# Kernel tuning notes

Hardware: AMD Instinct MI355X
Metric: run time of the kernel (lower is better)

The kernel has to match this reference:

```python
import jax, jax.numpy as jnp
import numpy as np

INPUT_DIM, HIDDEN_DIM, OUTPUT_DIM = 64, 256, 64
# AutoNCP(256, 64): inter_and_command=192, command=int(0.4*192)=76, inter=116, motor=64
INTER, COMMAND, MOTOR = 116, 76, 64
SENSORY_FANOUT, INTER_FANOUT, MOTOR_FANIN = 58, 38, 38
B, T = 512, 256


def setup_inputs() -> dict:
    rng = np.random.default_rng(0)
    key = jax.random.key(0)
    d = {}
    # NCP wiring sparsity (binary masks; ncps takes abs() so polarity is irrelevant for the mask)
    m0 = np.zeros((INTER, INPUT_DIM), np.float32)
    for i in range(INPUT_DIM):
        m0[rng.choice(INTER, SENSORY_FANOUT, replace=False), i] = 1.0
    m1 = np.zeros((COMMAND, INTER), np.float32)
    for i in range(INTER):
        m1[rng.choice(COMMAND, INTER_FANOUT, replace=False), i] = 1.0
    m2 = np.zeros((MOTOR, COMMAND), np.float32)
    for o in range(MOTOR):
        m2[o, rng.choice(COMMAND, MOTOR_FANIN, replace=False)] = 1.0
    dims = [(INPUT_DIM, INTER, m0), (INTER, COMMAND, m1), (COMMAND, MOTOR, m2)]
    for l, (fi, h, m) in enumerate(dims):
        cat = fi + h
        # mask shape [h, fi+h]: sparse prev-layer block + all-ones recurrent block (as in WiredCfCCell)
        d[f"mask_{l}"] = jnp.asarray(np.concatenate([m, np.ones((h, h), np.float32)], axis=1))
        bound = float(1.0 / np.sqrt(cat))
        for nm in ("ff1", "ff2", "ta", "tb"):
            key, k1, k2 = jax.random.split(key, 3)
            d[f"w_{nm}_{l}"] = jax.random.uniform(k1, (h, cat), minval=-bound, maxval=bound, dtype=jnp.float32)
            d[f"b_{nm}_{l}"] = jax.random.uniform(k2, (h,), minval=-bound, maxval=bound, dtype=jnp.float32)
    key, k1, k2, kx = jax.random.split(key, 4)
    bound = float(1.0 / np.sqrt(OUTPUT_DIM))
    d["w_fc"] = jax.random.uniform(k1, (OUTPUT_DIM, OUTPUT_DIM), minval=-bound, maxval=bound, dtype=jnp.float32)
    d["b_fc"] = jax.random.uniform(k2, (OUTPUT_DIM,), minval=-bound, maxval=bound, dtype=jnp.float32)
    d["x"] = jax.random.normal(kx, (B, T, INPUT_DIM), dtype=jnp.float32)
    return d


def _cfc_cell(xin, h, w1, b1, w2, b2, wa, ba, wb, bb, mask):
    # CfCCell 'default' mode, no backbone, ts = 1.0
    cat = jnp.concatenate([xin, h], axis=-1)          # [B, fi+h]
    ff1 = jnp.tanh(cat @ (w1 * mask).T + b1)
    ff2 = jnp.tanh(cat @ (w2 * mask).T + b2)
    t_interp = jax.nn.sigmoid(cat @ wa.T + ba + cat @ wb.T + bb)  # sigmoid(t_a*1.0 + t_b)
    return ff1 * (1.0 - t_interp) + t_interp * ff2


def _forward(x, layer_params, masks, w_fc, b_fc):
    bsz = x.shape[0]
    h0 = tuple(jnp.zeros((bsz, h), x.dtype) for h in (INTER, COMMAND, MOTOR))

    def step(hs, xt):
        inp = xt
        new = []
        for l in range(3):  # inter -> command -> motor (structurally distinct layers)
            h = _cfc_cell(inp, hs[l], *layer_params[l], masks[l])
            inp = h
            new.append(h)
        return tuple(new), inp  # motor-layer output per step

    _, ys = jax.lax.scan(step, h0, jnp.swapaxes(x, 0, 1))
    y = jnp.swapaxes(ys, 0, 1)  # [B, T, MOTOR]
    return y @ w_fc.T + b_fc


def reference(x, w_ff1_0, b_ff1_0, w_ff2_0, b_ff2_0, w_ta_0, b_ta_0, w_tb_0, b_tb_0,
              w_ff1_1, b_ff1_1, w_ff2_1, b_ff2_1, w_ta_1, b_ta_1, w_tb_1, b_tb_1,
              w_ff1_2, b_ff1_2, w_ff2_2, b_ff2_2, w_ta_2, b_ta_2, w_tb_2, b_tb_2,
              w_fc, b_fc, mask_0, mask_1, mask_2):
    layer_params = [
        (w_ff1_0, b_ff1_0, w_ff2_0, b_ff2_0, w_ta_0, b_ta_0, w_tb_0, b_tb_0),
        (w_ff1_1, b_ff1_1, w_ff2_1, b_ff2_1, w_ta_1, b_ta_1, w_tb_1, b_tb_1),
        (w_ff1_2, b_ff1_2, w_ff2_2, b_ff2_2, w_ta_2, b_ta_2, w_tb_2, b_tb_2),
    ]
    return _forward(x, layer_params, (mask_0, mask_1, mask_2), w_fc, b_fc)
```

## Files before the change

### kernel.cpp

```cpp
#include <hip/hip_runtime.h>

typedef _Float16 f16x8 __attribute__((ext_vector_type(8)));
typedef _Float16 f16x4 __attribute__((ext_vector_type(4)));
typedef _Float16 f16x2 __attribute__((ext_vector_type(2)));
typedef float f32x4 __attribute__((ext_vector_type(4)));

#define NTH 512
#define SEQT 256
#define LD0 200
#define LD1 200
#define LD2 168

struct KArgs { const float* in[30]; float* out; };

__device__ __forceinline__ float fast_tanh(float x) {
  return __fdividef(2.0f, 1.0f + __expf(-2.0f * x)) - 1.0f;
}
__device__ __forceinline__ float fast_sig(float x) {
  return __fdividef(1.0f, 1.0f + __expf(-x));
}

__device__ __forceinline__ f32x4 mfma16(f16x8 a, f16x8 b, f32x4 c) {
  return __builtin_amdgcn_mfma_f32_16x16x32_f16(a, b, c, 0, 0, 0);
}

__device__ __forceinline__ f16x4 combine3(const f32x4 acc[3]) {
  f16x4 v;
  #pragma unroll
  for (int q = 0; q < 4; ++q) {
    const float ff1 = fast_tanh(acc[0][q]);
    const float ff2 = fast_tanh(acc[1][q]);
    const float ti  = fast_sig(acc[2][q]);
    v[q] = (_Float16)(ff1 + ti * (ff2 - ff1));
  }
  return v;
}

template<int BASE, int KT>
__device__ __forceinline__ void load_tile(f16x8* wW, const float* W1, const float* W2,
                                          const float* Wa, const float* Wb,
                                          const float* Mk, int n, int CAT, int H, int kb) {
  #pragma unroll
  for (int kt = 0; kt < KT; ++kt) {
    #pragma unroll
    for (int m = 0; m < 3; ++m) {
      f16x8 f;
      #pragma unroll
      for (int j = 0; j < 8; ++j) {
        const int k = kt * 32 + kb + j;
        float v = 0.f;
        if (n < H && k < CAT) {
          if (m == 0)      v = W1[n*CAT+k] * Mk[n*CAT+k];
          else if (m == 1) v = W2[n*CAT+k] * Mk[n*CAT+k];
          else             v = Wa[n*CAT+k] + Wb[n*CAT+k];
        }
        f[j] = (_Float16)v;
      }
      wW[BASE + m*KT + kt] = f;
    }
  }
}

template<int KT>
__device__ __forceinline__ void loadB(f16x8* B, const _Float16* c, int LD, int r, int kb) {
  #pragma unroll
  for (int kt = 0; kt < KT; ++kt)
    B[kt] = *reinterpret_cast<const f16x8*>(c + r*LD + kt*32 + kb);
}

template<int BASE, int KT>
__device__ __forceinline__ void mma_tile(f32x4 acc[3], const f16x8* wW, const f16x8* B) {
  #pragma unroll
  for (int kt = 0; kt < KT; ++kt)
    #pragma unroll
    for (int m = 0; m < 3; ++m)
      acc[m] = mfma16(wW[BASE + m*KT + kt], B[kt], acc[m]);
}

__device__ __forceinline__ void init3(f32x4 acc[3], const float* sb, int bs, int n0) {
  #pragma unroll
  for (int m = 0; m < 3; ++m)
    acc[m] = *reinterpret_cast<const f32x4*>(sb + m*bs + n0);
}

__device__ __forceinline__ f16x8 loadB8u(const _Float16* p) {
  const f16x4 a = *reinterpret_cast<const f16x4*>(p);
  const f16x4 b = *reinterpret_cast<const f16x4*>(p + 4);
  f16x8 v;
  v[0]=a[0]; v[1]=a[1]; v[2]=a[2]; v[3]=a[3];
  v[4]=b[0]; v[5]=b[1]; v[6]=b[2]; v[7]=b[3];
  return v;
}

__global__ __launch_bounds__(NTH, 2) void ncp_fused(KArgs args) {
  __shared__ __align__(16) _Float16 c0[2][16 * LD0];
  __shared__ __align__(16) _Float16 c1[2][16 * LD1];
  __shared__ __align__(16) _Float16 c2[2][16 * LD2];
  __shared__ __align__(16) _Float16 wt3[15 * 64 * 8];
  __shared__ float b0s[3 * 128], b1s[3 * 80], b2s[3 * 64], bfcs[64];

  const int tid  = threadIdx.x;
  const int w    = tid >> 6;
  const int lane = tid & 63;
  const int r    = lane & 15;
  const int g    = lane >> 4;
  const int kb   = g * 8;
  const int wgBase = blockIdx.x * 16;
  const float* __restrict__ xg = args.in[29];

  f16x8 wW[37];
  if (w < 4) {
    load_tile<0, 6>(wW, args.in[1], args.in[3], args.in[5], args.in[7], args.in[0],
                    (2*w)*16 + r, 180, 116, kb);
    load_tile<18, 6>(wW, args.in[1], args.in[3], args.in[5], args.in[7], args.in[0],
                     (2*w+1)*16 + r, 180, 116, kb);
  } else if (w < 6) {
    load_tile<0, 6>(wW, args.in[10], args.in[12], args.in[14], args.in[16], args.in[9],
                    (2*(w-4))*16 + r, 192, 76, kb);
    load_tile<18, 6>(wW, args.in[10], args.in[12], args.in[14], args.in[16], args.in[9],
                     (2*(w-4)+1)*16 + r, 192, 76, kb);
  } else if (w == 6) {
    load_tile<0, 6>(wW, args.in[10], args.in[12], args.in[14], args.in[16], args.in[9],
                    64 + r, 192, 76, kb);
    load_tile<18, 5>(wW, args.in[19], args.in[21], args.in[23], args.in[25], args.in[18],
                     r, 140, 64, kb);
  } else {
    load_tile<0, 5>(wW, args.in[19], args.in[21], args.in[23], args.in[25], args.in[18],
                    16 + r, 140, 64, kb);
    load_tile<15, 5>(wW, args.in[19], args.in[21], args.in[23], args.in[25], args.in[18],
                     32 + r, 140, 64, kb);
  }
  if (w >= 6) {
    const int ot0 = (w - 6) * 2;
    #pragma unroll
    for (int tl = 0; tl < 2; ++tl)
      #pragma unroll
      for (int kt = 0; kt < 2; ++kt) {
        f16x8 f;
        #pragma unroll
        for (int j = 0; j < 8; ++j)
          f[j] = (_Float16)args.in[27][((ot0 + tl)*16 + r)*64 + kt*32 + kb + j];
        wW[33 + tl*2 + kt] = f;
      }
  }

  for (int u = tid; u < 15 * 64; u += NTH) {
    const int ln = u & 63;
    const int ff = u >> 6;
    const int kt = ff % 5, m = ff / 5;
    const int n  = 48 + (ln & 15);
    const int kbb = (ln >> 4) * 8;
    f16x8 f;
    #pragma unroll
    for (int j = 0; j < 8; ++j) {
      const int k = kt*32 + kbb + j;
      float v = 0.f;
      if (k < 140) {
        if (m == 0)      v = args.in[19][n*140+k] * args.in[18][n*140+k];
        else if (m == 1) v = args.in[21][n*140+k] * args.in[18][n*140+k];
        else             v = args.in[23][n*140+k] + args.in[25][n*140+k];
      }
      f[j] = (_Float16)v;
    }
    *reinterpret_cast<f16x8*>(wt3 + (size_t)u * 8) = f;
  }
  if (tid < 128) {
    b0s[tid]       = (tid < 116) ? args.in[2][tid] : 0.f;
    b0s[128 + tid] = (tid < 116) ? args.in[4][tid] : 0.f;
    b0s[256 + tid] = (tid < 116) ? args.in[6][tid] + args.in[8][tid] : 0.f;
  }
  if (tid < 80) {
    b1s[tid]       = (tid < 76) ? args.in[11][tid] : 0.f;
    b1s[80 + tid]  = (tid < 76) ? args.in[13][tid] : 0.f;
    b1s[160 + tid] = (tid < 76) ? args.in[15][tid] + args.in[17][tid] : 0.f;
  }
  if (tid < 64) {
    b2s[tid]       = args.in[20][tid];
    b2s[64 + tid]  = args.in[22][tid];
    b2s[128 + tid] = args.in[24][tid] + args.in[26][tid];
    bfcs[tid]      = args.in[28][tid];
  }
  for (int i = tid; i < 2 * 16 * LD0; i += NTH) c0[0][i] = (_Float16)0.f;
  for (int i = tid; i < 2 * 16 * LD1; i += NTH) c1[0][i] = (_Float16)0.f;
  for (int i = tid; i < 2 * 16 * LD2; i += NTH) c2[0][i] = (_Float16)0.f;
  __syncthreads();
  const int rr = tid >> 5, cc = (tid & 31) * 2;
  {
    const float2 v = *reinterpret_cast<const float2*>(
        xg + ((size_t)(wgBase + rr) * SEQT) * 64 + cc);
    f16x2 pk; pk[0] = (_Float16)v.x; pk[1] = (_Float16)v.y;
    *reinterpret_cast<f16x2*>(c0[0] + rr * LD0 + cc) = pk;
  }
  __syncthreads();

  const float* xp = xg + ((size_t)(wgBase + rr) * SEQT + 1) * 64 + cc;
  float* outp = args.out + ((size_t)(wgBase + r) * SEQT) * 64 + (w - 6) * 32 + 4 * g;

  #pragma unroll 1
  for (int p = 0; p < SEQT + 3; ++p) {
    const int cur = p & 1, nxt = cur ^ 1;

    float2 xv;
    const bool doX = (p < SEQT - 1);
    if (doX) xv = *reinterpret_cast<const float2*>(xp);

    if (w < 4) {
      if (p < SEQT) {
        f16x8 B[6]; loadB<6>(B, c0[cur], LD0, r, kb);
        f32x4 a[3];
        const int nA = (2*w)*16 + 4*g;
        init3(a, b0s, 128, nA);
        __builtin_amdgcn_s_setprio(1);
        mma_tile<0, 6>(a, wW, B);
        __builtin_amdgcn_s_setprio(0);
        const f16x4 vA = combine3(a);
        *reinterpret_cast<f16x4*>(c1[nxt] + r*LD1 + nA)      = vA;
        *reinterpret_cast<f16x4*>(c0[nxt] + r*LD0 + 64 + nA) = vA;
        const int nB = nA + 16;
        init3(a, b0s, 128, nB);
        __builtin_amdgcn_s_setprio(1);
        mma_tile<18, 6>(a, wW, B);
        __builtin_amdgcn_s_setprio(0);
        const f16x4 vB = combine3(a);
        if (nB < 116) {
          *reinterpret_cast<f16x4*>(c1[nxt] + r*LD1 + nB)      = vB;
          *reinterpret_cast<f16x4*>(c0[nxt] + r*LD0 + 64 + nB) = vB;
        }
      }
    } else if (w < 6) {
      if (p >= 1 && p <= SEQT) {
        f16x8 B[6]; loadB<6>(B, c1[cur], LD1, r, kb);
        f32x4 a[3];
        const int nA = (2*(w-4))*16 + 4*g;
        init3(a, b1s, 80, nA);
        __builtin_amdgcn_s_setprio(1);
        mma_tile<0, 6>(a, wW, B);
        __builtin_amdgcn_s_setprio(0);
        const f16x4 vA = combine3(a);
        *reinterpret_cast<f16x4*>(c1[nxt] + r*LD1 + 116 + nA) = vA;
        *reinterpret_cast<f16x4*>(c2[nxt] + r*LD2 + nA)       = vA;
        const int nB = nA + 16;
        init3(a, b1s, 80, nB);
        __builtin_amdgcn_s_setprio(1);
        mma_tile<18, 6>(a, wW, B);
        __builtin_amdgcn_s_setprio(0);
        const f16x4 vB = combine3(a);
        *reinterpret_cast<f16x4*>(c1[nxt] + r*LD1 + 116 + nB) = vB;
        *reinterpret_cast<f16x4*>(c2[nxt] + r*LD2 + nB)       = vB;
      }
    } else if (w == 6) {
      if (p >= 3) {
        f32x4 fa0 = *reinterpret_cast<const f32x4*>(bfcs + 4*g);
        f32x4 fa1 = *reinterpret_cast<const f32x4*>(bfcs + 16 + 4*g);
        const f16x8 hb0 = loadB8u(c2[cur] + r*LD2 + 76 + kb);
        const f16x8 hb1 = loadB8u(c2[cur] + r*LD2 + 76 + 32 + kb);
        fa0 = mfma16(wW[33], hb0, fa0); fa0 = mfma16(wW[34], hb1, fa0);
        fa1 = mfma16(wW[35], hb0, fa1); fa1 = mfma16(wW[36], hb1, fa1);
        *reinterpret_cast<f32x4*>(outp)      = fa0;
        *reinterpret_cast<f32x4*>(outp + 16) = fa1;
        outp += 64;
      }
      if (p >= 1 && p <= SEQT) {
        f16x8 B[6]; loadB<6>(B, c1[cur], LD1, r, kb);
        f32x4 a[3];
        const int n4 = 64 + 4*g;
        init3(a, b1s, 80, n4);
        __builtin_amdgcn_s_setprio(1);
        mma_tile<0, 6>(a, wW, B);
        __builtin_amdgcn_s_setprio(0);
        const f16x4 v4 = combine3(a);
        if (n4 < 76) {
          *reinterpret_cast<f16x4*>(c1[nxt] + r*LD1 + 116 + n4) = v4;
          *reinterpret_cast<f16x4*>(c2[nxt] + r*LD2 + n4)       = v4;
        }
      }
      if (p >= 2 && p <= SEQT + 1) {
        f16x8 B[5]; loadB<5>(B, c2[cur], LD2, r, kb);
        f32x4 a[3];
        const int nn = 4*g;
        init3(a, b2s, 64, nn);
        __builtin_amdgcn_s_setprio(1);
        mma_tile<18, 5>(a, wW, B);
        __builtin_amdgcn_s_setprio(0);
        const f16x4 v0 = combine3(a);
        *reinterpret_cast<f16x4*>(c2[nxt] + r*LD2 + 76 + nn) = v0;
      }
    } else {
      if (p >= 3) {
        f32x4 fa0 = *reinterpret_cast<const f32x4*>(bfcs + 32 + 4*g);
        f32x4 fa1 = *reinterpret_cast<const f32x4*>(bfcs + 48 + 4*g);
        const f16x8 hb0 = loadB8u(c2[cur] + r*LD2 + 76 + kb);
        const f16x8 hb1 = loadB8u(c2[cur] + r*LD2 + 76 + 32 + kb);
        fa0 = mfma16(wW[33], hb0, fa0); fa0 = mfma16(wW[34], hb1, fa0);
        fa1 = mfma16(wW[35], hb0, fa1); fa1 = mfma16(wW[36], hb1, fa1);
        *reinterpret_cast<f32x4*>(outp)      = fa0;
        *reinterpret_cast<f32x4*>(outp + 16) = fa1;
        outp += 64;
      }
      if (p >= 2 && p <= SEQT + 1) {
        f16x8 B[5]; loadB<5>(B, c2[cur], LD2, r, kb);
        f32x4 a[3];
        const int n1 = 16 + 4*g;
        init3(a, b2s, 64, n1);
        __builtin_amdgcn_s_setprio(1);
        mma_tile<0, 5>(a, wW, B);
        __builtin_amdgcn_s_setprio(0);
        const f16x4 v1 = combine3(a);
        *reinterpret_cast<f16x4*>(c2[nxt] + r*LD2 + 76 + n1) = v1;
        const int n2 = 32 + 4*g;
        init3(a, b2s, 64, n2);
        __builtin_amdgcn_s_setprio(1);
        mma_tile<15, 5>(a, wW, B);
        __builtin_amdgcn_s_setprio(0);
        const f16x4 v2 = combine3(a);
        *reinterpret_cast<f16x4*>(c2[nxt] + r*LD2 + 76 + n2) = v2;
        const int n3 = 48 + 4*g;
        init3(a, b2s, 64, n3);
        __builtin_amdgcn_s_setprio(1);
        #pragma unroll
        for (int kt = 0; kt < 5; ++kt) {
          #pragma unroll
          for (int m = 0; m < 3; ++m) {
            const f16x8 af = *reinterpret_cast<const f16x8*>(
                wt3 + (size_t)((m*5 + kt)*64 + lane) * 8);
            a[m] = mfma16(af, B[kt], a[m]);
          }
        }
        __builtin_amdgcn_s_setprio(0);
        const f16x4 v3 = combine3(a);
        *reinterpret_cast<f16x4*>(c2[nxt] + r*LD2 + 76 + n3) = v3;
      }
    }

    if (doX) {
      f16x2 pk; pk[0] = (_Float16)xv.x; pk[1] = (_Float16)xv.y;
      *reinterpret_cast<f16x2*>(c0[nxt] + rr * LD0 + cc) = pk;
      xp += 64;
    }
    __syncthreads();
  }
}

extern "C" void kernel_launch(void* const* d_in, const int* in_sizes, int n_in,
                              void* d_out, int out_size, void* d_ws, size_t ws_size,
                              hipStream_t stream) {
  KArgs args;
  for (int i = 0; i < 30; ++i) args.in[i] = (const float*)d_in[i];
  args.out = (float*)d_out;
  ncp_fused<<<dim3(32), dim3(NTH), 0, stream>>>(args);
}
```

Baseline: 810.9 us.

## Double workgroup to 16 waves, one output tile per wave

Raises the block size from 512 to 1024 threads so each wave computes a single 16-row output tile per layer instead of two. The per-wave register weight cache shrinks from 37 to 18 fragments, and the FC weights move into shared memory. The aim is to shorten the per-step critical path of the serial recurrence by spreading the MFMA and activation work across more waves. In exchange, each per-step barrier now synchronises twice as many waves, and the launch-bounds change raises the occupancy target.

Measured after the change: 712.7 us. 1.14x faster.

```diff
diff --git a/kernel.cpp b/kernel.cpp
--- a/kernel.cpp
+++ b/kernel.cpp
@@ -5,7 +5,7 @@
 typedef _Float16 f16x2 __attribute__((ext_vector_type(2)));
 typedef float f32x4 __attribute__((ext_vector_type(4)));
 
-#define NTH 512
+#define NTH 1024
 #define SEQT 256
 #define LD0 200
 #define LD1 200
@@ -36,7 +36,7 @@
   return v;
 }
 
-template<int BASE, int KT>
+template<int KT>
 __device__ __forceinline__ void load_tile(f16x8* wW, const float* W1, const float* W2,
                                           const float* Wa, const float* Wb,
                                           const float* Mk, int n, int CAT, int H, int kb) {
@@ -56,25 +56,22 @@
         }
         f[j] = (_Float16)v;
       }
-      wW[BASE + m*KT + kt] = f;
+      wW[m*KT + kt] = f;
     }
   }
 }
 
 template<int KT>
-__device__ __forceinline__ void loadB(f16x8* B, const _Float16* c, int LD, int r, int kb) {
-  #pragma unroll
-  for (int kt = 0; kt < KT; ++kt)
-    B[kt] = *reinterpret_cast<const f16x8*>(c + r*LD + kt*32 + kb);
-}
-
-template<int BASE, int KT>
-__device__ __forceinline__ void mma_tile(f32x4 acc[3], const f16x8* wW, const f16x8* B) {
-  #pragma unroll
-  for (int kt = 0; kt < KT; ++kt)
+__device__ __forceinline__ void mma_tile_ld(f32x4 acc[3], const f16x8* wW,
+                                            const _Float16* __restrict__ c,
+                                            int LD, int r, int kb) {
+  #pragma unroll
+  for (int kt = 0; kt < KT; ++kt) {
+    const f16x8 b = *reinterpret_cast<const f16x8*>(c + r*LD + kt*32 + kb);
     #pragma unroll
     for (int m = 0; m < 3; ++m)
-      acc[m] = mfma16(wW[BASE + m*KT + kt], B[kt], acc[m]);
+      acc[m] = mfma16(wW[m*KT + kt], b, acc[m]);
+  }
 }
 
 __device__ __forceinline__ void init3(f32x4 acc[3], const float* sb, int bs, int n0) {
@@ -92,15 +89,16 @@
   return v;
 }
 
-__global__ __launch_bounds__(NTH, 2) void ncp_fused(KArgs args) {
+__global__ __launch_bounds__(NTH, 4) void ncp_fused(KArgs args) {
   __shared__ __align__(16) _Float16 c0[2][16 * LD0];
   __shared__ __align__(16) _Float16 c1[2][16 * LD1];
   __shared__ __align__(16) _Float16 c2[2][16 * LD2];
   __shared__ __align__(16) _Float16 wt3[15 * 64 * 8];
+  __shared__ __align__(16) _Float16 wfcs[8 * 64 * 8];
   __shared__ float b0s[3 * 128], b1s[3 * 80], b2s[3 * 64], bfcs[64];
 
   const int tid  = threadIdx.x;
-  const int w    = tid >> 6;
+  const int wv   = tid >> 6;
   const int lane = tid & 63;
   const int r    = lane & 15;
   const int g    = lane >> 4;
@@ -108,40 +106,16 @@
   const int wgBase = blockIdx.x * 16;
   const float* __restrict__ xg = args.in[29];
 
-  f16x8 wW[37];
-  if (w < 4) {
-    load_tile<0, 6>(wW, args.in[1], args.in[3], args.in[5], args.in[7], args.in[0],
-                    (2*w)*16 + r, 180, 116, kb);
-    load_tile<18, 6>(wW, args.in[1], args.in[3], args.in[5], args.in[7], args.in[0],
-                     (2*w+1)*16 + r, 180, 116, kb);
-  } else if (w < 6) {
-    load_tile<0, 6>(wW, args.in[10], args.in[12], args.in[14], args.in[16], args.in[9],
-                    (2*(w-4))*16 + r, 192, 76, kb);
-    load_tile<18, 6>(wW, args.in[10], args.in[12], args.in[14], args.in[16], args.in[9],
-                     (2*(w-4)+1)*16 + r, 192, 76, kb);
-  } else if (w == 6) {
-    load_tile<0, 6>(wW, args.in[10], args.in[12], args.in[14], args.in[16], args.in[9],
-                    64 + r, 192, 76, kb);
-    load_tile<18, 5>(wW, args.in[19], args.in[21], args.in[23], args.in[25], args.in[18],
-                     r, 140, 64, kb);
+  f16x8 wW[18];
+  if (wv < 8) {
+    load_tile<6>(wW, args.in[1], args.in[3], args.in[5], args.in[7], args.in[0],
+                 wv*16 + r, 180, 116, kb);
+  } else if (wv < 13) {
+    load_tile<6>(wW, args.in[10], args.in[12], args.in[14], args.in[16], args.in[9],
+                 (wv-8)*16 + r, 192, 76, kb);
   } else {
-    load_tile<0, 5>(wW, args.in[19], args.in[21], args.in[23], args.in[25], args.in[18],
-                    16 + r, 140, 64, kb);
-    load_tile<15, 5>(wW, args.in[19], args.in[21], args.in[23], args.in[25], args.in[18],
-                     32 + r, 140, 64, kb);
-  }
-  if (w >= 6) {
-    const int ot0 = (w - 6) * 2;
-    #pragma unroll
-    for (int tl = 0; tl < 2; ++tl)
-      #pragma unroll
-      for (int kt = 0; kt < 2; ++kt) {
-        f16x8 f;
-        #pragma unroll
-        for (int j = 0; j < 8; ++j)
-          f[j] = (_Float16)args.in[27][((ot0 + tl)*16 + r)*64 + kt*32 + kb + j];
-        wW[33 + tl*2 + kt] = f;
-      }
+    load_tile<5>(wW, args.in[19], args.in[21], args.in[23], args.in[25], args.in[18],
+                 (wv-13)*16 + r, 140, 64, kb);
   }
 
   for (int u = tid; u < 15 * 64; u += NTH) {
@@ -164,6 +138,16 @@
     }
     *reinterpret_cast<f16x8*>(wt3 + (size_t)u * 8) = f;
   }
+  for (int u = tid; u < 8 * 64; u += NTH) {
+    const int ln = u & 63;
+    const int ff = u >> 6;
+    const int kt = ff & 1, ot = ff >> 1;
+    f16x8 f;
+    #pragma unroll
+    for (int j = 0; j < 8; ++j)
+      f[j] = (_Float16)args.in[27][(ot*16 + (ln & 15))*64 + kt*32 + (ln >> 4)*8 + j];
+    *reinterpret_cast<f16x8*>(wfcs + (size_t)u * 8) = f;
+  }
   if (tid < 128) {
     b0s[tid]       = (tid < 116) ? args.in[2][tid] : 0.f;
     b0s[128 + tid] = (tid < 116) ? args.in[4][tid] : 0.f;
@@ -184,8 +168,8 @@
   for (int i = tid; i < 2 * 16 * LD1; i += NTH) c1[0][i] = (_Float16)0.f;
   for (int i = tid; i < 2 * 16 * LD2; i += NTH) c2[0][i] = (_Float16)0.f;
   __syncthreads();
-  const int rr = tid >> 5, cc = (tid & 31) * 2;
-  {
+  const int rr = (tid & 511) >> 5, cc = (tid & 31) * 2;
+  if (tid < 512) {
     const float2 v = *reinterpret_cast<const float2*>(
         xg + ((size_t)(wgBase + rr) * SEQT) * 64 + cc);
     f16x2 pk; pk[0] = (_Float16)v.x; pk[1] = (_Float16)v.y;
@@ -194,141 +178,94 @@
   __syncthreads();
 
   const float* xp = xg + ((size_t)(wgBase + rr) * SEQT + 1) * 64 + cc;
-  float* outp = args.out + ((size_t)(wgBase + r) * SEQT) * 64 + (w - 6) * 32 + 4 * g;
+  const int otb = (wv >= 13) ? (wv - 13) : 0;
+  float* outp = args.out + ((size_t)(wgBase + r) * SEQT) * 64 + otb * 32 + 4 * g;
 
   #pragma unroll 1
   for (int p = 0; p < SEQT + 3; ++p) {
     const int cur = p & 1, nxt = cur ^ 1;
 
     float2 xv;
-    const bool doX = (p < SEQT - 1);
+    const bool doX = (tid < 512) && (p < SEQT - 1);
     if (doX) xv = *reinterpret_cast<const float2*>(xp);
 
-    if (w < 4) {
+    if (wv < 8) {
       if (p < SEQT) {
-        f16x8 B[6]; loadB<6>(B, c0[cur], LD0, r, kb);
         f32x4 a[3];
-        const int nA = (2*w)*16 + 4*g;
-        init3(a, b0s, 128, nA);
-        __builtin_amdgcn_s_setprio(1);
-        mma_tile<0, 6>(a, wW, B);
-        __builtin_amdgcn_s_setprio(0);
-        const f16x4 vA = combine3(a);
-        *reinterpret_cast<f16x4*>(c1[nxt] + r*LD1 + nA)      = vA;
-        *reinterpret_cast<f16x4*>(c0[nxt] + r*LD0 + 64 + nA) = vA;
-        const int nB = nA + 16;
-        init3(a, b0s, 128, nB);
-        __builtin_amdgcn_s_setprio(1);
-        mma_tile<18, 6>(a, wW, B);
-        __builtin_amdgcn_s_setprio(0);
-        const f16x4 vB = combine3(a);
-        if (nB < 116) {
-          *reinterpret_cast<f16x4*>(c1[nxt] + r*LD1 + nB)      = vB;
-          *reinterpret_cast<f16x4*>(c0[nxt] + r*LD0 + 64 + nB) = vB;
-        }
-      }
-    } else if (w < 6) {
+        const int nb = wv*16 + 4*g;
+        init3(a, b0s, 128, nb);
+        __builtin_amdgcn_s_setprio(1);
+        mma_tile_ld<6>(a, wW, c0[cur], LD0, r, kb);
+        __builtin_amdgcn_s_setprio(0);
+        const f16x4 v = combine3(a);
+        if (nb < 116) {
+          *reinterpret_cast<f16x4*>(c1[nxt] + r*LD1 + nb)      = v;
+          *reinterpret_cast<f16x4*>(c0[nxt] + r*LD0 + 64 + nb) = v;
+        }
+      }
+    } else if (wv < 13) {
       if (p >= 1 && p <= SEQT) {
-        f16x8 B[6]; loadB<6>(B, c1[cur], LD1, r, kb);
         f32x4 a[3];
-        const int nA = (2*(w-4))*16 + 4*g;
-        init3(a, b1s, 80, nA);
-        __builtin_amdgcn_s_setprio(1);
-        mma_tile<0, 6>(a, wW, B);
-        __builtin_amdgcn_s_setprio(0);
-        const f16x4 vA = combine3(a);
-        *reinterpret_cast<f16x4*>(c1[nxt] + r*LD1 + 116 + nA) = vA;
-        *reinterpret_cast<f16x4*>(c2[nxt] + r*LD2 + nA)       = vA;
-        const int nB = nA + 16;
-        init3(a, b1s, 80, nB);
-        __builtin_amdgcn_s_setprio(1);
-        mma_tile<18, 6>(a, wW, B);
-        __builtin_amdgcn_s_setprio(0);
-        const f16x4 vB = combine3(a);
-        *reinterpret_cast<f16x4*>(c1[nxt] + r*LD1 + 116 + nB) = vB;
-        *reinterpret_cast<f16x4*>(c2[nxt] + r*LD2 + nB)       = vB;
-      }
-    } else if (w == 6) {
+        const int nb = (wv-8)*16 + 4*g;
+        init3(a, b1s, 80, nb);
+        __builtin_amdgcn_s_setprio(1);
+        mma_tile_ld<6>(a, wW, c1[cur], LD1, r, kb);
+        __builtin_amdgcn_s_setprio(0);
+        const f16x4 v = combine3(a);
+        if (nb < 76) {
+          *reinterpret_cast<f16x4*>(c1[nxt] + r*LD1 + 116 + nb) = v;
+          *reinterpret_cast<f16x4*>(c2[nxt] + r*LD2 + nb)       = v;
+        }
+      }
+    } else if (wv < 15) {
       if (p >= 3) {
-        f32x4 fa0 = *reinterpret_cast<const f32x4*>(bfcs + 4*g);
-        f32x4 fa1 = *reinterpret_cast<const f32x4*>(bfcs + 16 + 4*g);
+        const int ot0 = (wv - 13) * 2;
+        f32x4 fa0 = *reinterpret_cast<const f32x4*>(bfcs + ot0*16 + 4*g);
+        f32x4 fa1 = *reinterpret_cast<const f32x4*>(bfcs + ot0*16 + 16 + 4*g);
         const f16x8 hb0 = loadB8u(c2[cur] + r*LD2 + 76 + kb);
         const f16x8 hb1 = loadB8u(c2[cur] + r*LD2 + 76 + 32 + kb);
-        fa0 = mfma16(wW[33], hb0, fa0); fa0 = mfma16(wW[34], hb1, fa0);
-        fa1 = mfma16(wW[35], hb0, fa1); fa1 = mfma16(wW[36], hb1, fa1);
+        const f16x8 wf00 = *reinterpret_cast<const f16x8*>(wfcs + (size_t)((ot0*2    )*64 + lane)*8);
+        const f16x8 wf01 = *reinterpret_cast<const f16x8*>(wfcs + (size_t)((ot0*2 + 1)*64 + lane)*8);
+        const f16x8 wf10 = *reinterpret_cast<const f16x8*>(wfcs + (size_t)((ot0*2 + 2)*64 + lane)*8);
+        const f16x8 wf11 = *reinterpret_cast<const f16x8*>(wfcs + (size_t)((ot0*2 + 3)*64 + lane)*8);
+        fa0 = mfma16(wf00, hb0, fa0); fa0 = mfma16(wf01, hb1, fa0);
+        fa1 = mfma16(wf10, hb0, fa1); fa1 = mfma16(wf11, hb1, fa1);
         *reinterpret_cast<f32x4*>(outp)      = fa0;
         *reinterpret_cast<f32x4*>(outp + 16) = fa1;
         outp += 64;
       }
-      if (p >= 1 && p <= SEQT) {
-        f16x8 B[6]; loadB<6>(B, c1[cur], LD1, r, kb);
+      if (p >= 2 && p <= SEQT + 1) {
         f32x4 a[3];
-        const int n4 = 64 + 4*g;
-        init3(a, b1s, 80, n4);
-        __builtin_amdgcn_s_setprio(1);
-        mma_tile<0, 6>(a, wW, B);
-        __builtin_amdgcn_s_setprio(0);
-        const f16x4 v4 = combine3(a);
-        if (n4 < 76) {
-          *reinterpret_cast<f16x4*>(c1[nxt] + r*LD1 + 116 + n4) = v4;
-          *reinterpret_cast<f16x4*>(c2[nxt] + r*LD2 + n4)       = v4;
-        }
-      }
+        const int nb = (wv-13)*16 + 4*g;
+        init3(a, b2s, 64, nb);
+        __builtin_amdgcn_s_setprio(1);
+        mma_tile_ld<5>(a, wW, c2[cur], LD2, r, kb);
+        __builtin_amdgcn_s_setprio(0);
+        const f16x4 v = combine3(a);
+        *reinterpret_cast<f16x4*>(c2[nxt] + r*LD2 + 76 + nb) = v;
+      }
+    } else {
       if (p >= 2 && p <= SEQT + 1) {
-        f16x8 B[5]; loadB<5>(B, c2[cur], LD2, r, kb);
-        f32x4 a[3];
-        const int nn = 4*g;
-        init3(a, b2s, 64, nn);
-        __builtin_amdgcn_s_setprio(1);
-        mma_tile<18, 5>(a, wW, B);
-        __builtin_amdgcn_s_setprio(0);
-        const f16x4 v0 = combine3(a);
-        *reinterpret_cast<f16x4*>(c2[nxt] + r*LD2 + 76 + nn) = v0;
-      }
-    } else {
-      if (p >= 3) {
-        f32x4 fa0 = *reinterpret_cast<const f32x4*>(bfcs + 32 + 4*g);
-        f32x4 fa1 = *reinterpret_cast<const f32x4*>(bfcs + 48 + 4*g);
-        const f16x8 hb0 = loadB8u(c2[cur] + r*LD2 + 76 + kb);
-        const f16x8 hb1 = loadB8u(c2[cur] + r*LD2 + 76 + 32 + kb);
-        fa0 = mfma16(wW[33], hb0, fa0); fa0 = mfma16(wW[34], hb1, fa0);
-        fa1 = mfma16(wW[35], hb0, fa1); fa1 = mfma16(wW[36], hb1, fa1);
-        *reinterpret_cast<f32x4*>(outp)      = fa0;
-        *reinterpret_cast<f32x4*>(outp + 16) = fa1;
-        outp += 64;
-      }
-      if (p >= 2 && p <= SEQT + 1) {
-        f16x8 B[5]; loadB<5>(B, c2[cur], LD2, r, kb);
-        f32x4 a[3];
-        const int n1 = 16 + 4*g;
-        init3(a, b2s, 64, n1);
-        __builtin_amdgcn_s_setprio(1);
-        mma_tile<0, 5>(a, wW, B);
-        __builtin_amdgcn_s_setprio(0);
-        const f16x4 v1 = combine3(a);
-        *reinterpret_cast<f16x4*>(c2[nxt] + r*LD2 + 76 + n1) = v1;
-        const int n2 = 32 + 4*g;
-        init3(a, b2s, 64, n2);
-        __builtin_amdgcn_s_setprio(1);
-        mma_tile<15, 5>(a, wW, B);
-        __builtin_amdgcn_s_setprio(0);
-        const f16x4 v2 = combine3(a);
-        *reinterpret_cast<f16x4*>(c2[nxt] + r*LD2 + 76 + n2) = v2;
-        const int n3 = 48 + 4*g;
-        init3(a, b2s, 64, n3);
+        f32x4 a2[3], a3[3];
+        init3(a2, b2s, 64, 32 + 4*g);
+        init3(a3, b2s, 64, 48 + 4*g);
         __builtin_amdgcn_s_setprio(1);
         #pragma unroll
         for (int kt = 0; kt < 5; ++kt) {
+          const f16x8 b = *reinterpret_cast<const f16x8*>(c2[cur] + r*LD2 + kt*32 + kb);
           #pragma unroll
           for (int m = 0; m < 3; ++m) {
+            a2[m] = mfma16(wW[m*5 + kt], b, a2[m]);
             const f16x8 af = *reinterpret_cast<const f16x8*>(
                 wt3 + (size_t)((m*5 + kt)*64 + lane) * 8);
-            a[m] = mfma16(af, B[kt], a[m]);
+            a3[m] = mfma16(af, b, a3[m]);
           }
         }
         __builtin_amdgcn_s_setprio(0);
-        const f16x4 v3 = combine3(a);
-        *reinterpret_cast<f16x4*>(c2[nxt] + r*LD2 + 76 + n3) = v3;
+        const f16x4 v2 = combine3(a2);
+        const f16x4 v3 = combine3(a3);
+        *reinterpret_cast<f16x4*>(c2[nxt] + r*LD2 + 76 + 32 + 4*g) = v2;
+        *reinterpret_cast<f16x4*>(c2[nxt] + r*LD2 + 76 + 48 + 4*g) = v3;
       }
     }
 
```
